# Optimization experiments

Hardware: AMD Instinct MI355X
Metric: run time of the kernel (lower is better)

## Reference

```python
import jax, jax.numpy as jnp
import numpy as np

B, S, E, H = 2, 2048, 1024, 16
D = E // H
THETA = 10000.0


def _rope_cos_sin():
    # Faithful to source: freqs_cis is indexed by input_shape[1], which after
    # _split_heads is the HEAD dimension, so 'positions' are head indices 0..H-1.
    freqs = 1.0 / (THETA ** (jnp.arange(0, D, 2, dtype=jnp.float32) / D))  # [D/2]
    pos = jnp.arange(H, dtype=jnp.float32)  # head indices (source bug, reproduced)
    ang = jnp.outer(pos, freqs)  # [H, D/2]
    # broadcast shape [1, H, 1, D/2] against [B, H, S, D/2]
    return jnp.cos(ang)[None, :, None, :], jnp.sin(ang)[None, :, None, :]


def _apply_rope(x, cos, sin):
    # x: [B, H, S, D]; complex pairs are (even, odd) along last dim
    xe, xo = x[..., 0::2], x[..., 1::2]
    re = xe * cos - xo * sin
    im = xe * sin + xo * cos
    # interleave back: view_as_real(...).flatten(3)
    return jnp.stack([re, im], axis=-1).reshape(x.shape)


def setup_inputs() -> dict:
    key = jax.random.key(0)
    ks = jax.random.split(key, 5)
    s = 0.02
    return {
        "hidden_states": jax.random.normal(ks[0], (B, S, E), dtype=jnp.float32),
        "W_attn": jax.random.normal(ks[1], (E, 3 * E), dtype=jnp.float32) * s,
        "b_attn": jnp.zeros((3 * E,), dtype=jnp.float32),
        "W_proj": jax.random.normal(ks[2], (E, E), dtype=jnp.float32) * s,
        "b_proj": jnp.zeros((E,), dtype=jnp.float32),
    }


def reference(hidden_states, W_attn, b_attn, W_proj, b_proj):
    qkv = hidden_states @ W_attn + b_attn  # [B, S, 3E]
    q, k, v = jnp.split(qkv, 3, axis=-1)
    # split heads -> [B, H, S, D]
    def split_heads(t):
        return t.reshape(B, S, H, D).transpose(0, 2, 1, 3)
    q, k, v = split_heads(q), split_heads(k), split_heads(v)
    cos, sin = _rope_cos_sin()
    q = _apply_rope(q, cos, sin)
    k = _apply_rope(k, cos, sin)
    scores = jnp.einsum("bhqd,bhkd->bhqk", q, k) / jnp.sqrt(jnp.float32(D))
    causal = jnp.tril(jnp.ones((S, S), dtype=bool))
    neg = jnp.finfo(scores.dtype).min
    scores = jnp.where(causal[None, None], scores, neg)
    attn = jax.nn.softmax(scores, axis=-1)
    out = jnp.einsum("bhqk,bhkd->bhqd", attn, v)  # [B, H, S, D]
    out = out.transpose(0, 2, 1, 3).reshape(B, S, E)  # merge heads
    return out @ W_proj + b_proj
```

## Files before the change

### kernel.cpp

```cpp
#include <hip/hip_runtime.h>
#include <hip/hip_bf16.h>
#include <cstdint>
#include <cstddef>


typedef float  f32x4 __attribute__((ext_vector_type(4)));
typedef __bf16 bf16x8 __attribute__((ext_vector_type(8)));

__device__ __forceinline__ unsigned short f2bf(float f) {
  union { __bf16 b; unsigned short u; } c; c.b = (__bf16)f; return c.u;
}
__device__ __forceinline__ unsigned short bf2u(__bf16 b) {
  union { __bf16 b; unsigned short u; } c; c.b = b; return c.u;
}

__device__ __forceinline__ void gload_lds16(const void* g, void* l) {
  __builtin_amdgcn_global_load_lds(
      (const __attribute__((address_space(1))) unsigned int*)g,
      (__attribute__((address_space(3))) unsigned int*)l, 16, 0, 0);
}

__global__ __launch_bounds__(256) void cast_x_k(const float* __restrict__ in,
                                                __bf16* __restrict__ out) {
  size_t i = (size_t)blockIdx.x * 256 + threadIdx.x;
  f32x4 a = *(const f32x4*)(in + i * 8);
  f32x4 b = *(const f32x4*)(in + i * 8 + 4);
  bf16x8 o;
  o[0]=(__bf16)a[0]; o[1]=(__bf16)a[1]; o[2]=(__bf16)a[2]; o[3]=(__bf16)a[3];
  o[4]=(__bf16)b[0]; o[5]=(__bf16)b[1]; o[6]=(__bf16)b[2]; o[7]=(__bf16)b[3];
  *(bf16x8*)(out + i * 8) = o;
}

template<bool ROPE>
__global__ __launch_bounds__(256) void transpose_rot_k(const float* __restrict__ W,
                                                       __bf16* __restrict__ Wt,
                                                       int Kd, int Nd) {
  __shared__ float tile[32][33];
  const int tx = threadIdx.x, ty = threadIdx.y;
  const int n0 = blockIdx.x * 32, k0 = blockIdx.y * 32;
#pragma unroll
  for (int i = 0; i < 4; i++)
    tile[ty + 8 * i][tx] = W[(size_t)(k0 + ty + 8 * i) * Nd + n0 + tx];
  __syncthreads();
#pragma unroll
  for (int i = 0; i < 4; i++) {
    int nl = ty + 8 * i;
    int n  = n0 + nl;
    float v;
    if (ROPE && n < 2048) {
      int nn = n & 1023;
      int h = nn >> 6, d = nn & 63, ip = d >> 1;
      float ang = (float)h * powf(10000.0f, -(float)ip / 32.0f);
      float s, c; sincosf(ang, &s, &c);
      float xe = tile[tx][nl & ~1], xo = tile[tx][nl | 1];
      v = (d & 1) ? (xe * s + xo * c) : (xe * c - xo * s);
    } else {
      v = tile[tx][nl];
    }
    Wt[(size_t)n * Kd + k0 + tx] = (__bf16)v;
  }
}

__global__ __launch_bounds__(256) void rot_bias_k(const float* __restrict__ b,
                                                  float* __restrict__ out) {
  int n = blockIdx.x * 256 + threadIdx.x;
  if (n < 3072) {
    float v;
    if (n < 2048) {
      int nn = n & 1023, h = nn >> 6, d = nn & 63, ip = d >> 1;
      float ang = (float)h * powf(10000.0f, -(float)ip / 32.0f);
      float s, c; sincosf(ang, &s, &c);
      float xe = b[n & ~1], xo = b[n | 1];
      v = (d & 1) ? (xe * s + xo * c) : (xe * c - xo * s);
    } else v = b[n];
    out[n] = v;
  }
}

template<int MODE, int BN>
__global__ __launch_bounds__(256) void gemm_bt_k(
    const __bf16* __restrict__ A, const __bf16* __restrict__ Bt,
    const float* __restrict__ bias, float* __restrict__ outf,
    __bf16* __restrict__ Qo, __bf16* __restrict__ Ko, __bf16* __restrict__ Vo,
    int M, int N, int K)
{
  constexpr int MI = (BN == 128) ? 4 : 2;
  __shared__ __align__(16) char Asm[2][8192];
  __shared__ __align__(16) char Bsm[2][BN * 64];
  const int tid = threadIdx.x;
  const int m0 = blockIdx.y * 128, n0 = blockIdx.x * BN;
  const int wid = tid >> 6, lane = tid & 63;
  const int wr = (BN == 128) ? (wid >> 1) : wid;
  const int wc = (BN == 128) ? (wid & 1) : 0;
  const int li = lane & 15, gq = lane >> 4;

  const f32x4 fzero = {0.f, 0.f, 0.f, 0.f};
  f32x4 acc[MI][4];
#pragma unroll
  for (int i = 0; i < MI; i++)
#pragma unroll
    for (int j = 0; j < 4; j++) acc[i][j] = fzero;

  const int NT = K >> 5;

  auto stage = [&](int buf, int kt) {
    const int ko = kt * 32;
#pragma unroll
    for (int it = 0; it < 2; it++) {
      const int idx = wid * 128 + it * 64 + lane;
      const int row = idx >> 2, cb = idx & 3;
      gload_lds16(A + (size_t)(m0 + row) * K + ko + cb * 8,
                  Asm[buf] + (size_t)(wid * 128 + it * 64) * 16);
    }
    if constexpr (BN == 128) {
#pragma unroll
      for (int it = 0; it < 2; it++) {
        const int idx = wid * 128 + it * 64 + lane;
        const int row = idx >> 2, cb = idx & 3;
        gload_lds16(Bt + (size_t)(n0 + row) * K + ko + cb * 8,
                    Bsm[buf] + (size_t)(wid * 128 + it * 64) * 16);
      }
    } else {
      const int row = tid >> 2, cb = tid & 3;
      gload_lds16(Bt + (size_t)(n0 + row) * K + ko + cb * 8,
                  Bsm[buf] + (size_t)(wid * 64) * 16);
    }
  };

  stage(0, 0);
  __syncthreads();
  int cur = 0;

  for (int kt = 0; kt < NT; ++kt) {
    if (kt + 1 < NT) stage(cur ^ 1, kt + 1);
    bf16x8 af[MI], bfr[4];
#pragma unroll
    for (int mi = 0; mi < MI; mi++)
      af[mi] = *(const bf16x8*)(Asm[cur] + (wr * (MI * 16) + mi * 16 + li) * 64 + gq * 16);
#pragma unroll
    for (int ni = 0; ni < 4; ni++)
      bfr[ni] = *(const bf16x8*)(Bsm[cur] + (wc * 64 + ni * 16 + li) * 64 + gq * 16);
#pragma unroll
    for (int mi = 0; mi < MI; mi++)
#pragma unroll
      for (int ni = 0; ni < 4; ni++)
        acc[mi][ni] = __builtin_amdgcn_mfma_f32_16x16x32_bf16(af[mi], bfr[ni],
                                                              acc[mi][ni], 0, 0, 0);
    __syncthreads();
    cur ^= 1;
  }

#pragma unroll
  for (int ni = 0; ni < 4; ni++) {
    const int n = n0 + wc * 64 + ni * 16 + li;
    const float bv = bias[n];
#pragma unroll
    for (int mi = 0; mi < MI; mi++) {
#pragma unroll
      for (int r = 0; r < 4; r++) {
        const int m = m0 + wr * (MI * 16) + mi * 16 + 4 * gq + r;
        const float val = acc[mi][ni][r] + bv;
        if (MODE == 0) {
          const int region = n >> 10, nn = n & 1023;
          const int h = nn >> 6, d = nn & 63;
          const int b = m >> 11, s = m & 2047;
          __bf16* dst = (region == 0) ? Qo : (region == 1) ? Ko : Vo;
          dst[(((size_t)(b * 16 + h)) * 2048 + s) * 64 + d] = (__bf16)val;
        } else {
          outf[(size_t)m * N + n] = val;
        }
      }
    }
  }
}

__global__ __launch_bounds__(256) void attn_k(
    const __bf16* __restrict__ Q, const __bf16* __restrict__ K,
    const __bf16* __restrict__ V, __bf16* __restrict__ O)
{
  __shared__ __align__(16) char Ksm[2][8192];
  __shared__ __align__(16) char Vsm[2][8192];
  __shared__ __align__(16) char Psm[4][2048];
  const int pr = blockIdx.x, bh = blockIdx.y;
  const int qta = pr, qtb = 31 - pr;
  const int NTa = qta + 1;
  const int NT  = NTa + qtb + 1;
  const int tid = threadIdx.x, wid = tid >> 6, lane = tid & 63;
  const int li = lane & 15, gq = lane >> 4;
  const size_t base = (size_t)bh * 2048 * 64;
  const int swz = (li & 7) << 4;
  const f32x4 fzero = {0.f, 0.f, 0.f, 0.f};
  const float SC = 0.18033688011f;

  const int rowa = qta * 64 + wid * 16 + li;
  const int rowb = qtb * 64 + wid * 16 + li;
  bf16x8 qfa[2], qfb[2], qcur[2];
#pragma unroll
  for (int kc = 0; kc < 2; kc++) {
    qfa[kc] = *(const bf16x8*)(Q + base + (size_t)rowa * 64 + kc * 32 + gq * 8);
    qfb[kc] = *(const bf16x8*)(Q + base + (size_t)rowb * 64 + kc * 32 + gq * 8);
  }
  qcur[0] = qfa[0]; qcur[1] = qfa[1];

  f32x4 o[4];
#pragma unroll
  for (int dn = 0; dn < 4; dn++) o[dn] = fzero;
  float mrun = -1e30f, lrun = 0.f;
  int iq = rowa;
  char* pw = Psm[wid];
  const int b = bh >> 4, h = bh & 15;

  auto epilogue = [&](int qt) {
#pragma unroll
    for (int r = 0; r < 4; r++) {
      float lr  = __shfl(lrun, 4 * gq + r);
      float inv = 1.0f / lr;
      int qrow = qt * 64 + wid * 16 + 4 * gq + r;
#pragma unroll
      for (int dn = 0; dn < 4; dn++) {
        O[((size_t)(b * 2048 + qrow)) * 1024 + h * 64 + dn * 16 + li] =
            (__bf16)(o[dn][r] * inv);
      }
    }
  };

  const bool roleK = (wid < 2);
  const int st = tid & 127;
  const int vkk = (st >> 3) * 4, vd0 = (st & 7) * 8;
  f32x4 kreg[4];
  bf16x8 vreg[4];

  auto loadTile = [&](int ko) {
    if (roleK) {
#pragma unroll
      for (int t = 0; t < 4; t++) {
        const int ci = st + 128 * t;
        const int row = ci >> 3, cb = ci & 7;
        kreg[t] = *(const f32x4*)(K + base + (size_t)(ko + row) * 64 + cb * 8);
      }
    } else {
#pragma unroll
      for (int u = 0; u < 4; u++)
        vreg[u] = *(const bf16x8*)(V + base + (size_t)(ko + vkk + u) * 64 + vd0);
    }
  };
  auto writeTile = [&](int buf) {
    if (roleK) {
#pragma unroll
      for (int t = 0; t < 4; t++) {
        const int ci = st + 128 * t;
        const int row = ci >> 3, cb = ci & 7;
        *(f32x4*)(Ksm[buf] + ((row * 128 + cb * 16) ^ ((row & 7) << 4))) = kreg[t];
      }
    } else {
#pragma unroll
      for (int j = 0; j < 8; j++) {
        const int d = vd0 + j;
        uint2 w;
        w.x = (unsigned)bf2u(vreg[0][j]) | ((unsigned)bf2u(vreg[1][j]) << 16);
        w.y = (unsigned)bf2u(vreg[2][j]) | ((unsigned)bf2u(vreg[3][j]) << 16);
        *(uint2*)(Vsm[buf] + ((d * 128 + vkk * 2) ^ ((d & 7) << 4))) = w;
      }
    }
  };

  auto kofs = [&](int i) { return (i < NTa ? i : i - NTa) * 64; };

  loadTile(kofs(0));
  writeTile(0);
  loadTile(kofs(1));
  __syncthreads();

  for (int i = 0; i < NT; ++i) {
    const int cur = i & 1;
    if (i + 1 < NT) writeTile(cur ^ 1);
    if (i + 2 < NT) loadTile(kofs(i + 2));

    if (i == NTa) {
      epilogue(qta);
#pragma unroll
      for (int dn = 0; dn < 4; dn++) o[dn] = fzero;
      mrun = -1e30f; lrun = 0.f;
      iq = rowb;
      qcur[0] = qfb[0]; qcur[1] = qfb[1];
    }
    const bool diag = (i == NTa - 1) || (i == NT - 1);
    const int kbase = kofs(i);

    f32x4 s4[4];
#pragma unroll
    for (int f = 0; f < 4; f++) s4[f] = fzero;
#pragma unroll
    for (int kc = 0; kc < 2; kc++) {
#pragma unroll
      for (int f = 0; f < 4; f++) {
        bf16x8 kf = *(const bf16x8*)(Ksm[cur] +
            (((f * 16 + li) * 128 + kc * 64 + gq * 16) ^ swz));
        s4[f] = __builtin_amdgcn_mfma_f32_16x16x32_bf16(kf, qcur[kc], s4[f], 0, 0, 0);
      }
    }
    float p[4][4];
    float tmax = -1e30f;
    if (diag) {
#pragma unroll
      for (int f = 0; f < 4; f++)
#pragma unroll
        for (int r = 0; r < 4; r++) {
          float sv = s4[f][r] * SC;
          int j = kbase + f * 16 + 4 * gq + r;
          if (j > iq) sv = -1e30f;
          p[f][r] = sv;
          tmax = fmaxf(tmax, sv);
        }
    } else {
#pragma unroll
      for (int f = 0; f < 4; f++)
#pragma unroll
        for (int r = 0; r < 4; r++) {
          float sv = s4[f][r] * SC;
          p[f][r] = sv;
          tmax = fmaxf(tmax, sv);
        }
    }
    tmax = fmaxf(tmax, __shfl_xor(tmax, 16));
    tmax = fmaxf(tmax, __shfl_xor(tmax, 32));
    if (!__all(tmax - mrun <= 11.0f)) {
      float mnew  = fmaxf(mrun, tmax);
      float alpha = exp2f(mrun - mnew);
#pragma unroll
      for (int r = 0; r < 4; r++) {
        float ar = __shfl(alpha, 4 * gq + r);
#pragma unroll
        for (int dn = 0; dn < 4; dn++) o[dn][r] *= ar;
      }
      lrun *= alpha;
      mrun = mnew;
    }
    float ts = 0.f;
#pragma unroll
    for (int f = 0; f < 4; f++)
#pragma unroll
      for (int r = 0; r < 4; r++) {
        float pv = exp2f(p[f][r] - mrun);
        p[f][r] = pv;
        ts += pv;
      }
    ts += __shfl_xor(ts, 16);
    ts += __shfl_xor(ts, 32);
    lrun += ts;
#pragma unroll
    for (int f = 0; f < 4; f++) {
      unsigned lo = (unsigned)f2bf(p[f][0]) | ((unsigned)f2bf(p[f][1]) << 16);
      unsigned hi = (unsigned)f2bf(p[f][2]) | ((unsigned)f2bf(p[f][3]) << 16);
      uint2 w2; w2.x = lo; w2.y = hi;
      *(uint2*)(pw + ((li * 128 + f * 32 + gq * 8) ^ swz)) = w2;
    }
#pragma unroll
    for (int kc = 0; kc < 2; kc++) {
      bf16x8 paf = *(const bf16x8*)(pw + ((li * 128 + kc * 64 + gq * 16) ^ swz));
#pragma unroll
      for (int dn = 0; dn < 4; dn++) {
        bf16x8 vb = *(const bf16x8*)(Vsm[cur] +
            (((dn * 16 + li) * 128 + kc * 64 + gq * 16) ^ swz));
        o[dn] = __builtin_amdgcn_mfma_f32_16x16x32_bf16(paf, vb, o[dn], 0, 0, 0);
      }
    }

    __syncthreads();
  }

  epilogue(qtb);
}

extern "C" void kernel_launch(void* const* d_in, const int* in_sizes, int n_in,
                              void* d_out, int out_size, void* d_ws, size_t ws_size,
                              hipStream_t stream) {
  const float* hidden = (const float*)d_in[0];
  const float* W_attn = (const float*)d_in[1];
  const float* b_attn = (const float*)d_in[2];
  const float* W_proj = (const float*)d_in[3];
  const float* b_proj = (const float*)d_in[4];
  float* out = (float*)d_out;

  char* ws = (char*)d_ws;
  size_t off = 0;
  auto alloc = [&](size_t bytes) -> char* {
    char* p = ws + off;
    off += (bytes + 255) & ~(size_t)255;
    return p;
  };
  __bf16* Xb  = (__bf16*)alloc((size_t)4096 * 1024 * 2);
  __bf16* Wat = (__bf16*)alloc((size_t)3072 * 1024 * 2);
  __bf16* Wpt = (__bf16*)alloc((size_t)1024 * 1024 * 2);
  float*  ba  = (float*) alloc((size_t)3072 * 4);
  __bf16* Qb  = (__bf16*)alloc((size_t)32 * 2048 * 64 * 2);
  __bf16* Kb  = (__bf16*)alloc((size_t)32 * 2048 * 64 * 2);
  __bf16* Vb  = (__bf16*)alloc((size_t)32 * 2048 * 64 * 2);
  __bf16* Ob  = (__bf16*)alloc((size_t)4096 * 1024 * 2);

  cast_x_k<<<2048, 256, 0, stream>>>(hidden, Xb);
  transpose_rot_k<true ><<<dim3(96, 32), dim3(32, 8), 0, stream>>>(W_attn, Wat, 1024, 3072);
  transpose_rot_k<false><<<dim3(32, 32), dim3(32, 8), 0, stream>>>(W_proj, Wpt, 1024, 1024);
  rot_bias_k<<<12, 256, 0, stream>>>(b_attn, ba);

  gemm_bt_k<0, 128><<<dim3(24, 32), 256, 0, stream>>>(Xb, Wat, ba, nullptr,
                                                      Qb, Kb, Vb, 4096, 3072, 1024);
  attn_k<<<dim3(16, 32), 256, 0, stream>>>(Qb, Kb, Vb, Ob);
  gemm_bt_k<1, 64><<<dim3(16, 32), 256, 0, stream>>>(Ob, Wpt, b_proj, out,
                                                     nullptr, nullptr, nullptr,
                                                     4096, 1024, 1024);
}
```

Measured before the change: 219.8 us.

## Widen attention KV tiles to 128 keys and remap blocks across XCDs

The attention kernel now processes 128-key K/V tiles per iteration instead of 64, so each query-tile pair runs a fixed 17 iterations. This halves the number of loop trips and barriers and enlarges the LDS buffers, at the cost of more registers and more masked work on diagonal tiles. Both the GEMM and attention kernels remap block IDs in a round-robin pattern across the chiplet groups to improve cache locality. s_setprio is raised around the MFMA sections to favour matrix-issue waves.

```diff
diff --git a/kernel.cpp b/kernel.cpp
--- a/kernel.cpp
+++ b/kernel.cpp
@@ -6,6 +6,7 @@
 
 typedef float  f32x4 __attribute__((ext_vector_type(4)));
 typedef __bf16 bf16x8 __attribute__((ext_vector_type(8)));
+typedef unsigned int u32x4 __attribute__((ext_vector_type(4)));
 
 __device__ __forceinline__ unsigned short f2bf(float f) {
   union { __bf16 b; unsigned short u; } c; c.b = (__bf16)f; return c.u;
@@ -88,7 +89,11 @@
   __shared__ __align__(16) char Asm[2][8192];
   __shared__ __align__(16) char Bsm[2][BN * 64];
   const int tid = threadIdx.x;
-  const int m0 = blockIdx.y * 128, n0 = blockIdx.x * BN;
+  const int gx = gridDim.x;
+  const int orig = blockIdx.y * gx + blockIdx.x;
+  const int cpx = (gx * gridDim.y) >> 3;
+  const int wk = (orig & 7) * cpx + (orig >> 3);
+  const int m0 = (wk / gx) * 128, n0 = (wk % gx) * BN;
   const int wid = tid >> 6, lane = tid & 63;
   const int wr = (BN == 128) ? (wid >> 1) : wid;
   const int wc = (BN == 128) ? (wid & 1) : 0;
@@ -178,13 +183,15 @@
     const __bf16* __restrict__ Q, const __bf16* __restrict__ K,
     const __bf16* __restrict__ V, __bf16* __restrict__ O)
 {
-  __shared__ __align__(16) char Ksm[2][8192];
-  __shared__ __align__(16) char Vsm[2][8192];
-  __shared__ __align__(16) char Psm[4][2048];
-  const int pr = blockIdx.x, bh = blockIdx.y;
+  __shared__ __align__(16) char Ksm[2][16384];
+  __shared__ __align__(16) char Vsm[2][16384];
+  __shared__ __align__(16) char Psm[4][4096];
+  const int orig = blockIdx.y * 16 + blockIdx.x;
+  const int wkid = (orig & 7) * 64 + (orig >> 3);
+  const int pr = wkid & 15, bh = wkid >> 4;
   const int qta = pr, qtb = 31 - pr;
-  const int NTa = qta + 1;
-  const int NT  = NTa + qtb + 1;
+  const int Ta = (qta >> 1) + 1;
+  const int NT = 17;
   const int tid = threadIdx.x, wid = tid >> 6, lane = tid & 63;
   const int li = lane & 15, gq = lane >> 4;
   const size_t base = (size_t)bh * 2048 * 64;
@@ -226,45 +233,44 @@
 
   const bool roleK = (wid < 2);
   const int st = tid & 127;
-  const int vkk = (st >> 3) * 4, vd0 = (st & 7) * 8;
-  f32x4 kreg[4];
-  bf16x8 vreg[4];
+  const int krow0 = st >> 3, kcb = st & 7;
+  const int vkk = (st >> 3) * 8, vd0 = (st & 7) * 8;
+  f32x4 kreg[8];
+  bf16x8 vreg[8];
 
   auto loadTile = [&](int ko) {
     if (roleK) {
 #pragma unroll
-      for (int t = 0; t < 4; t++) {
-        const int ci = st + 128 * t;
-        const int row = ci >> 3, cb = ci & 7;
-        kreg[t] = *(const f32x4*)(K + base + (size_t)(ko + row) * 64 + cb * 8);
-      }
+      for (int t = 0; t < 8; t++)
+        kreg[t] = *(const f32x4*)(K + base + (size_t)(ko + krow0 + 16 * t) * 64 + kcb * 8);
     } else {
 #pragma unroll
-      for (int u = 0; u < 4; u++)
+      for (int u = 0; u < 8; u++)
         vreg[u] = *(const bf16x8*)(V + base + (size_t)(ko + vkk + u) * 64 + vd0);
     }
   };
   auto writeTile = [&](int buf) {
     if (roleK) {
 #pragma unroll
-      for (int t = 0; t < 4; t++) {
-        const int ci = st + 128 * t;
-        const int row = ci >> 3, cb = ci & 7;
-        *(f32x4*)(Ksm[buf] + ((row * 128 + cb * 16) ^ ((row & 7) << 4))) = kreg[t];
+      for (int t = 0; t < 8; t++) {
+        const int row = krow0 + 16 * t;
+        *(f32x4*)(Ksm[buf] + ((row * 128 + kcb * 16) ^ ((row & 7) << 4))) = kreg[t];
       }
     } else {
 #pragma unroll
       for (int j = 0; j < 8; j++) {
         const int d = vd0 + j;
-        uint2 w;
-        w.x = (unsigned)bf2u(vreg[0][j]) | ((unsigned)bf2u(vreg[1][j]) << 16);
-        w.y = (unsigned)bf2u(vreg[2][j]) | ((unsigned)bf2u(vreg[3][j]) << 16);
-        *(uint2*)(Vsm[buf] + ((d * 128 + vkk * 2) ^ ((d & 7) << 4))) = w;
+        u32x4 wv;
+        wv[0] = (unsigned)bf2u(vreg[0][j]) | ((unsigned)bf2u(vreg[1][j]) << 16);
+        wv[1] = (unsigned)bf2u(vreg[2][j]) | ((unsigned)bf2u(vreg[3][j]) << 16);
+        wv[2] = (unsigned)bf2u(vreg[4][j]) | ((unsigned)bf2u(vreg[5][j]) << 16);
+        wv[3] = (unsigned)bf2u(vreg[6][j]) | ((unsigned)bf2u(vreg[7][j]) << 16);
+        *(u32x4*)(Vsm[buf] + ((d * 256 + vkk * 2) ^ ((d & 7) << 4))) = wv;
       }
     }
   };
 
-  auto kofs = [&](int i) { return (i < NTa ? i : i - NTa) * 64; };
+  auto kofs = [&](int i) { return (i < Ta ? i : i - Ta) * 128; };
 
   loadTile(kofs(0));
   writeTile(0);
@@ -276,7 +282,7 @@
     if (i + 1 < NT) writeTile(cur ^ 1);
     if (i + 2 < NT) loadTile(kofs(i + 2));
 
-    if (i == NTa) {
+    if (i == Ta) {
       epilogue(qta);
 #pragma unroll
       for (int dn = 0; dn < 4; dn++) o[dn] = fzero;
@@ -284,41 +290,42 @@
       iq = rowb;
       qcur[0] = qfb[0]; qcur[1] = qfb[1];
     }
-    const bool diag = (i == NTa - 1) || (i == NT - 1);
+    const bool diag = (i == Ta - 1) || (i == NT - 1);
     const int kbase = kofs(i);
 
-    f32x4 s4[4];
-#pragma unroll
-    for (int f = 0; f < 4; f++) s4[f] = fzero;
+    f32x4 s4[8];
+#pragma unroll
+    for (int f = 0; f < 8; f++) s4[f] = fzero;
+    __builtin_amdgcn_s_setprio(1);
 #pragma unroll
     for (int kc = 0; kc < 2; kc++) {
 #pragma unroll
-      for (int f = 0; f < 4; f++) {
+      for (int f = 0; f < 8; f++) {
         bf16x8 kf = *(const bf16x8*)(Ksm[cur] +
             (((f * 16 + li) * 128 + kc * 64 + gq * 16) ^ swz));
         s4[f] = __builtin_amdgcn_mfma_f32_16x16x32_bf16(kf, qcur[kc], s4[f], 0, 0, 0);
       }
     }
-    float p[4][4];
+    __builtin_amdgcn_s_setprio(0);
     float tmax = -1e30f;
     if (diag) {
 #pragma unroll
-      for (int f = 0; f < 4; f++)
+      for (int f = 0; f < 8; f++)
 #pragma unroll
         for (int r = 0; r < 4; r++) {
           float sv = s4[f][r] * SC;
           int j = kbase + f * 16 + 4 * gq + r;
           if (j > iq) sv = -1e30f;
-          p[f][r] = sv;
+          s4[f][r] = sv;
           tmax = fmaxf(tmax, sv);
         }
     } else {
 #pragma unroll
-      for (int f = 0; f < 4; f++)
+      for (int f = 0; f < 8; f++)
 #pragma unroll
         for (int r = 0; r < 4; r++) {
           float sv = s4[f][r] * SC;
-          p[f][r] = sv;
+          s4[f][r] = sv;
           tmax = fmaxf(tmax, sv);
         }
     }
@@ -338,33 +345,35 @@
     }
     float ts = 0.f;
 #pragma unroll
-    for (int f = 0; f < 4; f++)
+    for (int f = 0; f < 8; f++)
 #pragma unroll
       for (int r = 0; r < 4; r++) {
-        float pv = exp2f(p[f][r] - mrun);
-        p[f][r] = pv;
+        float pv = exp2f(s4[f][r] - mrun);
+        s4[f][r] = pv;
         ts += pv;
       }
     ts += __shfl_xor(ts, 16);
     ts += __shfl_xor(ts, 32);
     lrun += ts;
 #pragma unroll
-    for (int f = 0; f < 4; f++) {
-      unsigned lo = (unsigned)f2bf(p[f][0]) | ((unsigned)f2bf(p[f][1]) << 16);
-      unsigned hi = (unsigned)f2bf(p[f][2]) | ((unsigned)f2bf(p[f][3]) << 16);
+    for (int f = 0; f < 8; f++) {
+      unsigned lo = (unsigned)f2bf(s4[f][0]) | ((unsigned)f2bf(s4[f][1]) << 16);
+      unsigned hi = (unsigned)f2bf(s4[f][2]) | ((unsigned)f2bf(s4[f][3]) << 16);
       uint2 w2; w2.x = lo; w2.y = hi;
-      *(uint2*)(pw + ((li * 128 + f * 32 + gq * 8) ^ swz)) = w2;
-    }
-#pragma unroll
-    for (int kc = 0; kc < 2; kc++) {
-      bf16x8 paf = *(const bf16x8*)(pw + ((li * 128 + kc * 64 + gq * 16) ^ swz));
+      *(uint2*)(pw + ((li * 256 + f * 32 + gq * 8) ^ swz)) = w2;
+    }
+    __builtin_amdgcn_s_setprio(1);
+#pragma unroll
+    for (int kc = 0; kc < 4; kc++) {
+      bf16x8 paf = *(const bf16x8*)(pw + ((li * 256 + kc * 64 + gq * 16) ^ swz));
 #pragma unroll
       for (int dn = 0; dn < 4; dn++) {
         bf16x8 vb = *(const bf16x8*)(Vsm[cur] +
-            (((dn * 16 + li) * 128 + kc * 64 + gq * 16) ^ swz));
+            (((dn * 16 + li) * 256 + kc * 64 + gq * 16) ^ swz));
         o[dn] = __builtin_amdgcn_mfma_f32_16x16x32_bf16(paf, vb, o[dn], 0, 0, 0);
       }
     }
+    __builtin_amdgcn_s_setprio(0);
 
     __syncthreads();
   }
```

New measurement: 244.3 us. 11.2% more time.
